# Kernel optimization log

Hardware: AMD Instinct MI355X
Metric: run time of the kernel (lower is better)

Reference implementation:

```python
import jax, jax.numpy as jnp
import numpy as np

EPS = 1e-8


def setup_inputs() -> dict:
    key = jax.random.key(0)
    k1, k2, k3, k4 = jax.random.split(key, 4)
    B, Cin, Cout, K, S, H, W = 8, 512, 512, 3, 512, 64, 64
    return {
        "x": jax.random.normal(k1, (B, Cin, H, W), dtype=jnp.float32),
        "style": jax.random.normal(k2, (B, S), dtype=jnp.float32),
        "weight": jax.random.normal(k3, (1, Cout, Cin, K, K), dtype=jnp.float32),
        "mod_w": jax.random.normal(k4, (Cin, S), dtype=jnp.float32),
        "mod_b": jnp.ones((Cin,), dtype=jnp.float32),
    }


def reference(x, style, weight, mod_w, mod_b):
    B, Cin, H, W = x.shape
    Cout, K = weight.shape[1], weight.shape[-1]
    style_dim = mod_w.shape[1]
    conv_scale = 1.0 / np.sqrt(Cin * K * K)  # 1/sqrt(fan_in)
    mod_scale = 1.0 / np.sqrt(style_dim)     # EqualLinear scale (lr_mul=1)

    # EqualLinear modulation: (B, Cin)
    s = style @ (mod_w * mod_scale).T + mod_b

    # per-sample modulated weights: (B, Cout, Cin, K, K)
    w = conv_scale * weight * s[:, None, :, None, None]
    demod = jax.lax.rsqrt(jnp.sum(w * w, axis=(2, 3, 4)) + EPS)  # (B, Cout)
    w = w * demod[:, :, None, None, None]

    # grouped conv with groups = batch
    w = w.reshape(B * Cout, Cin, K, K)
    xg = x.reshape(1, B * Cin, H, W)
    pad = (K - 1) // 2
    out = jax.lax.conv_general_dilated(
        xg, w,
        window_strides=(1, 1),
        padding=[(pad, pad), (pad, pad)],
        dimension_numbers=("NCHW", "OIHW", "NCHW"),
        feature_group_count=B,
    )
    return out.reshape(B, Cout, out.shape[2], out.shape[3])
```

## Files before the change

### kernel.cpp

```cpp
#include <hip/hip_runtime.h>
#include <hip/hip_bf16.h>
#include <cstdint>
#include <cstddef>

typedef __bf16 bf16x8 __attribute__((ext_vector_type(8)));
typedef float f32x4 __attribute__((ext_vector_type(4)));
typedef unsigned int uintx4 __attribute__((ext_vector_type(4)));

#define CONV_SCALE 0.014731391274719738f
#define MOD_SCALE  0.044194173824159216f

__device__ __forceinline__ unsigned short f2bf(float v) {
  unsigned int u = __float_as_uint(v);
  return (unsigned short)((u + 0x7FFFu + ((u >> 16) & 1u)) >> 16);
}

__device__ __forceinline__ void gload16(const void* g, void* l) {
  __builtin_amdgcn_global_load_lds(
      (const __attribute__((address_space(1))) unsigned int*)g,
      (__attribute__((address_space(3))) unsigned int*)l, 16, 0, 0);
}

__global__ void k_modulate(const float* __restrict__ style,
                           const float* __restrict__ mod_w,
                           const float* __restrict__ mod_b,
                           float* __restrict__ s) {
  int blk = blockIdx.x;
  int b = blk >> 2, ch = blk & 3;
  int t = threadIdx.x;
  int ci = ch * 128 + (t >> 1), half = t & 1;
  const float* st = style + b * 512 + half * 256;
  const float* mw = mod_w + (size_t)ci * 512 + half * 256;
  float acc = 0.f;
  #pragma unroll 8
  for (int k = 0; k < 256; k += 4) {
    f32x4 a = *(const f32x4*)(st + k);
    f32x4 m = *(const f32x4*)(mw + k);
    acc += a[0] * m[0] + a[1] * m[1] + a[2] * m[2] + a[3] * m[3];
  }
  acc += __shfl_xor(acc, 1);
  if (half == 0) s[b * 512 + ci] = acc * MOD_SCALE + mod_b[ci];
}

__global__ void k_wTq(const float* __restrict__ weight,
                      unsigned short* __restrict__ wT,
                      float* __restrict__ wsq) {
  __shared__ float lds[4608];
  int co = blockIdx.x;
  int t = threadIdx.x;
  const float* w = weight + (size_t)co * 4608;
  #pragma unroll
  for (int i = 0; i < 18; ++i) lds[t + i * 256] = w[t + i * 256];
  __syncthreads();
  for (int i = t; i < 576; i += 256) {
    int tap = i / 64, c8 = (i & 63) * 8;
    union { uintx4 v; unsigned short us[8]; } pk;
    #pragma unroll
    for (int j = 0; j < 8; ++j) pk.us[j] = f2bf(lds[(c8 + j) * 9 + tap]);
    *(uintx4*)(wT + ((size_t)tap * 512 + co) * 512 + c8) = pk.v;
  }
  for (int ci = t; ci < 512; ci += 256) {
    float a = 0.f;
    #pragma unroll
    for (int tap = 0; tap < 9; ++tap) { float v = lds[ci * 9 + tap]; a += v * v; }
    wsq[co * 512 + ci] = a * (CONV_SCALE * CONV_SCALE);
  }
}

__global__ void k_demod(const float* __restrict__ wsq, const float* __restrict__ s,
                        float* __restrict__ demod) {
  int b = blockIdx.x;
  int co = threadIdx.x;
  const float* wq = wsq + (size_t)co * 512;
  const float* sb = s + b * 512;
  float acc = 0.f;
  #pragma unroll 4
  for (int ci = 0; ci < 512; ci += 4) {
    f32x4 q = *(const f32x4*)(wq + ci);
    f32x4 v = *(const f32x4*)(sb + ci);
    acc += q[0] * v[0] * v[0] + q[1] * v[1] * v[1] + q[2] * v[2] * v[2] + q[3] * v[3] * v[3];
  }
  demod[b * 512 + co] = rsqrtf(acc + 1e-8f);
}

__global__ void k_xT(const float* __restrict__ x, const float* __restrict__ s,
                     unsigned short* __restrict__ xT) {
  __shared__ float lds[128][68];
  int cc = blockIdx.x;
  int h = blockIdx.y;
  int b = blockIdx.z;
  int t = threadIdx.x;
  int w4 = (t & 15) * 4, rr = t >> 4;
  #pragma unroll
  for (int i = 0; i < 8; ++i) {
    int ci = i * 16 + rr;
    *(f32x4*)&lds[ci][w4] =
        *(const f32x4*)&x[(((size_t)(b * 512 + cc * 128 + ci)) * 64 + h) * 64 + w4];
  }
  __syncthreads();
  int pos = t >> 2, c4 = t & 3;
  #pragma unroll
  for (int q = 0; q < 4; ++q) {
    int cb = q * 32 + c4 * 8;
    union { uintx4 v; unsigned short us[8]; } pk;
    #pragma unroll
    for (int j = 0; j < 8; ++j) {
      int ci = cb + j;
      pk.us[j] = f2bf(lds[ci][pos] * s[b * 512 + cc * 128 + ci]);
    }
    *(uintx4*)(xT + (((size_t)(b * 64 + h)) * 64 + pos) * 512 + cc * 128 + cb) = pk.v;
  }
}

__global__ __launch_bounds__(256, 2) void k_conv(
    const unsigned short* __restrict__ xT,
    const unsigned short* __restrict__ wT,
    const float* __restrict__ demod,
    float* __restrict__ out) {
  extern __shared__ __align__(16) char lds_raw[];
  char* xlds = lds_raw;
  char* wlds = lds_raw + 42240;

  const int co_t = blockIdx.x;
  const int h_t  = blockIdx.y;
  const int b    = blockIdx.z;
  const int t = threadIdx.x;
  const int lane = t & 63, wv = t >> 6;
  const int h0 = h_t * 8;
  const int co0 = co_t * 64;
  const int l15 = lane & 15, kg = lane >> 4;

  {
    uintx4 z = {0u, 0u, 0u, 0u};
    for (int i = t; i < 2640; i += 256) ((uintx4*)xlds)[i] = z;
  }

  f32x4 acc[4][2][4] = {};

  for (int cc = 0; cc < 16; ++cc) {
    __syncthreads();
    for (int j = wv; j < 40; j += 4) {
      int r = j >> 2, k = j & 3;
      int hh = h0 - 1 + r;
      if ((unsigned)hh < 64u) {
        int p0 = r * 66 + 1 + k * 16;
        int p = p0 + (lane >> 2);
        const unsigned short* g = xT + (((size_t)(b * 64 + hh)) * 64 + k * 16 + (lane >> 2)) * 512
                                  + cc * 32 + (((lane & 3) ^ ((p >> 1) & 3)) << 3);
        gload16(g, xlds + p0 * 64);
      }
    }
    for (int j = wv; j < 36; j += 4) {
      int row0 = j * 16;
      int row = row0 + (lane >> 2);
      int tap = row >> 6, co = row & 63;
      const unsigned short* g = wT + ((size_t)tap * 512 + co0 + co) * 512
                                + cc * 32 + (((lane & 3) ^ ((row >> 1) & 3)) << 3);
      gload16(g, wlds + row0 * 64);
    }
    __syncthreads();

    #pragma unroll
    for (int tap = 0; tap < 9; ++tap) {
      const int dh = tap / 3, dw = tap % 3;
      bf16x8 af[4], bfr[2][4];
      #pragma unroll
      for (int m = 0; m < 4; ++m) {
        int row = tap * 64 + m * 16 + l15;
        af[m] = *(const bf16x8*)(wlds + row * 64 + ((kg ^ ((row >> 1) & 3)) << 4));
      }
      #pragma unroll
      for (int r = 0; r < 2; ++r)
        #pragma unroll
        for (int n = 0; n < 4; ++n) {
          int p = (2 * wv + r + dh) * 66 + n * 16 + l15 + dw;
          bfr[r][n] = *(const bf16x8*)(xlds + p * 64 + ((kg ^ ((p >> 1) & 3)) << 4));
        }
      #pragma unroll
      for (int m = 0; m < 4; ++m)
        #pragma unroll
        for (int r = 0; r < 2; ++r)
          #pragma unroll
          for (int n = 0; n < 4; ++n)
            acc[m][r][n] = __builtin_amdgcn_mfma_f32_16x16x32_bf16(af[m], bfr[r][n], acc[m][r][n], 0, 0, 0);
    }
  }

  #pragma unroll
  for (int m = 0; m < 4; ++m) {
    #pragma unroll
    for (int q = 0; q < 4; ++q) {
      int co = co0 + m * 16 + kg * 4 + q;
      float scl = CONV_SCALE * demod[b * 512 + co];
      #pragma unroll
      for (int r = 0; r < 2; ++r) {
        int h_out = h0 + 2 * wv + r;
        #pragma unroll
        for (int n = 0; n < 4; ++n) {
          out[(((size_t)(b * 512 + co)) * 64 + h_out) * 64 + n * 16 + l15] = acc[m][r][n][q] * scl;
        }
      }
    }
  }
}

extern "C" void kernel_launch(void* const* d_in, const int* in_sizes, int n_in,
                              void* d_out, int out_size, void* d_ws, size_t ws_size,
                              hipStream_t stream) {
  const float* x      = (const float*)d_in[0];
  const float* style  = (const float*)d_in[1];
  const float* weight = (const float*)d_in[2];
  const float* mod_w  = (const float*)d_in[3];
  const float* mod_b  = (const float*)d_in[4];
  float* out = (float*)d_out;

  char* ws = (char*)d_ws;
  unsigned short* xT = (unsigned short*)ws;
  unsigned short* wT = (unsigned short*)(ws + 33554432);
  float* s     = (float*)(ws + 38273024);
  float* wsq   = (float*)(ws + 38289408);
  float* demod = (float*)(ws + 39337984);

  static int lds_set = 0;
  if (!lds_set) {
    (void)hipFuncSetAttribute((const void*)k_conv,
                              hipFuncAttributeMaxDynamicSharedMemorySize, 79104);
    lds_set = 1;
  }

  hipLaunchKernelGGL(k_modulate, dim3(32),       dim3(256), 0, stream, style, mod_w, mod_b, s);
  hipLaunchKernelGGL(k_wTq,      dim3(512),      dim3(256), 0, stream, weight, wT, wsq);
  hipLaunchKernelGGL(k_demod,    dim3(8),        dim3(512), 0, stream, wsq, s, demod);
  hipLaunchKernelGGL(k_xT,       dim3(4, 64, 8), dim3(256), 0, stream, x, s, xT);
  hipLaunchKernelGGL(k_conv,     dim3(8, 8, 8),  dim3(256), 79104, stream, xT, wT, demod, out);
}
```

Before: 193.9 us.

## Double-buffer conv tiles with register-staged prefetch and larger row tiles

The conv kernel now uses 512 threads covering 16 output rows per block, which halves the grid in h and doubles reuse of each weight tile. The next channel chunk is prefetched while the current one computes: x goes through registers and is written to LDS after compute, and weights are loaded asynchronously into a second LDS buffer. MFMA work runs at raised wave priority. LDS per block grows to about 146 KB, so only one block fits per CU despite the launch bound of two. Register pressure also rises from the nine staged x vectors, and the grid shrinks to 256 blocks.

```diff
diff --git a/kernel.cpp b/kernel.cpp
--- a/kernel.cpp
+++ b/kernel.cpp
@@ -112,54 +112,85 @@
   }
 }
 
-__global__ __launch_bounds__(256, 2) void k_conv(
+__global__ __launch_bounds__(512, 2) void k_conv(
     const unsigned short* __restrict__ xT,
     const unsigned short* __restrict__ wT,
     const float* __restrict__ demod,
     float* __restrict__ out) {
   extern __shared__ __align__(16) char lds_raw[];
   char* xlds = lds_raw;
-  char* wlds = lds_raw + 42240;
+  char* wlds = lds_raw + 76032;
 
   const int co_t = blockIdx.x;
   const int h_t  = blockIdx.y;
   const int b    = blockIdx.z;
   const int t = threadIdx.x;
   const int lane = t & 63, wv = t >> 6;
-  const int h0 = h_t * 8;
+  const int h0 = h_t * 16;
   const int co0 = co_t * 64;
   const int l15 = lane & 15, kg = lane >> 4;
 
   {
     uintx4 z = {0u, 0u, 0u, 0u};
-    for (int i = t; i < 2640; i += 256) ((uintx4*)xlds)[i] = z;
-  }
-
-  f32x4 acc[4][2][4] = {};
-
-  for (int cc = 0; cc < 16; ++cc) {
-    __syncthreads();
-    for (int j = wv; j < 40; j += 4) {
-      int r = j >> 2, k = j & 3;
-      int hh = h0 - 1 + r;
-      if ((unsigned)hh < 64u) {
-        int p0 = r * 66 + 1 + k * 16;
-        int p = p0 + (lane >> 2);
-        const unsigned short* g = xT + (((size_t)(b * 64 + hh)) * 64 + k * 16 + (lane >> 2)) * 512
-                                  + cc * 32 + (((lane & 3) ^ ((p >> 1) & 3)) << 3);
-        gload16(g, xlds + p0 * 64);
-      }
-    }
-    for (int j = wv; j < 36; j += 4) {
+    for (int i = t; i < 4752; i += 512) ((uintx4*)xlds)[i] = z;
+  }
+
+  const int slot = t & 3;
+  const int c    = (t >> 2) & 63;
+  const int rb   = t >> 8;
+  unsigned xgo[9]; unsigned xlo[9]; bool xv[9];
+  #pragma unroll
+  for (int k = 0; k < 9; ++k) {
+    int r = 2 * k + rb;
+    int hh = h0 - 1 + r;
+    xv[k] = ((unsigned)hh < 64u);
+    int p = r * 66 + 1 + c;
+    xlo[k] = p * 64 + ((slot ^ ((p >> 1) & 3)) << 4);
+    xgo[k] = ((unsigned)((b * 64 + (xv[k] ? hh : 0)) * 64 + c) << 10) + slot * 16;
+  }
+  const char* xTb = (const char*)xT;
+  uintx4 xr[9] = {};
+
+  auto xissue = [&](int ccn) {
+    unsigned off = ccn * 64;
+    #pragma unroll
+    for (int k = 0; k < 9; ++k)
+      if (xv[k]) xr[k] = *(const uintx4*)(xTb + xgo[k] + off);
+  };
+  auto xwrite = [&]() {
+    #pragma unroll
+    for (int k = 0; k < 9; ++k) *(uintx4*)(xlds + xlo[k]) = xr[k];
+  };
+  auto wissue = [&](int ccn, char* wb) {
+    for (int j = wv; j < 36; j += 8) {
       int row0 = j * 16;
       int row = row0 + (lane >> 2);
       int tap = row >> 6, co = row & 63;
       const unsigned short* g = wT + ((size_t)tap * 512 + co0 + co) * 512
-                                + cc * 32 + (((lane & 3) ^ ((row >> 1) & 3)) << 3);
-      gload16(g, wlds + row0 * 64);
-    }
-    __syncthreads();
-
+                                + ccn * 32 + (((lane & 3) ^ ((row >> 1) & 3)) << 3);
+      gload16(g, wb + row0 * 64);
+    }
+  };
+
+  f32x4 acc[4][2][4] = {};
+
+  char* wb0 = wlds;
+  char* wb1 = wlds + 36864;
+
+  xissue(0);
+  wissue(0, wb0);
+  xwrite();
+  __syncthreads();
+
+  #pragma unroll 1
+  for (int cc = 0; cc < 16; ++cc) {
+    char* wb = (cc & 1) ? wb1 : wb0;
+    if (cc < 15) {
+      xissue(cc + 1);
+      wissue(cc + 1, (cc & 1) ? wb0 : wb1);
+      __builtin_amdgcn_sched_barrier(0);
+    }
+    __builtin_amdgcn_s_setprio(1);
     #pragma unroll
     for (int tap = 0; tap < 9; ++tap) {
       const int dh = tap / 3, dw = tap % 3;
@@ -167,7 +198,7 @@
       #pragma unroll
       for (int m = 0; m < 4; ++m) {
         int row = tap * 64 + m * 16 + l15;
-        af[m] = *(const bf16x8*)(wlds + row * 64 + ((kg ^ ((row >> 1) & 3)) << 4));
+        af[m] = *(const bf16x8*)(wb + row * 64 + ((kg ^ ((row >> 1) & 3)) << 4));
       }
       #pragma unroll
       for (int r = 0; r < 2; ++r)
@@ -183,6 +214,12 @@
           #pragma unroll
           for (int n = 0; n < 4; ++n)
             acc[m][r][n] = __builtin_amdgcn_mfma_f32_16x16x32_bf16(af[m], bfr[r][n], acc[m][r][n], 0, 0, 0);
+    }
+    __builtin_amdgcn_s_setprio(0);
+    if (cc < 15) {
+      __syncthreads();
+      xwrite();
+      __syncthreads();
     }
   }
 
@@ -224,7 +261,7 @@
   static int lds_set = 0;
   if (!lds_set) {
     (void)hipFuncSetAttribute((const void*)k_conv,
-                              hipFuncAttributeMaxDynamicSharedMemorySize, 79104);
+                              hipFuncAttributeMaxDynamicSharedMemorySize, 149760);
     lds_set = 1;
   }
 
@@ -232,5 +269,5 @@
   hipLaunchKernelGGL(k_wTq,      dim3(512),      dim3(256), 0, stream, weight, wT, wsq);
   hipLaunchKernelGGL(k_demod,    dim3(8),        dim3(512), 0, stream, wsq, s, demod);
   hipLaunchKernelGGL(k_xT,       dim3(4, 64, 8), dim3(256), 0, stream, x, s, xT);
-  hipLaunchKernelGGL(k_conv,     dim3(8, 8, 8),  dim3(256), 79104, stream, xT, wT, demod, out);
-}
+  hipLaunchKernelGGL(k_conv,     dim3(8, 4, 8),  dim3(512), 149760, stream, xT, wT, demod, out);
+}
```

Result: slower. 269.6 us (+39.1%).

## Double-buffer conv input tiles and ring-buffer weights with 512-thread blocks

Applied to the files above, without the earlier changes.

Restructures the implicit-GEMM conv kernel into a software pipeline. The input tile is double-buffered, and weights stream per tap through a 4-slot LDS ring, with loads issued two taps ahead and gated by vmcnt waits instead of full barriers around each channel chunk. Blocks grow to 512 threads covering 128 output channels, which doubles input-tile reuse. A 1D grid reorders blocks by output-channel group, and s_setprio is raised around MFMA bursts. LDS use rises to about 118KB per block, which may limit occupancy to one block per CU. The hand-placed waitcnt counts and barrier placement are fragile.

```diff
diff --git a/kernel.cpp b/kernel.cpp
--- a/kernel.cpp
+++ b/kernel.cpp
@@ -112,70 +112,105 @@
   }
 }
 
-__global__ __launch_bounds__(256, 2) void k_conv(
+__global__ __launch_bounds__(512, 2) void k_conv(
     const unsigned short* __restrict__ xT,
     const unsigned short* __restrict__ wT,
     const float* __restrict__ demod,
     float* __restrict__ out) {
   extern __shared__ __align__(16) char lds_raw[];
-  char* xlds = lds_raw;
-  char* wlds = lds_raw + 42240;
-
-  const int co_t = blockIdx.x;
-  const int h_t  = blockIdx.y;
-  const int b    = blockIdx.z;
+  char* xb0   = lds_raw;
+  char* xb1   = lds_raw + 42240;
+  char* wring = lds_raw + 84480;
+  char* trash = lds_raw + 117248;
+
+  const int id  = blockIdx.x;
+  const int g_ord = (id & 7) * 32 + (id >> 3);
+  const int co_t  = g_ord >> 6;
+  const int slice = g_ord & 63;
+  const int b   = slice >> 3;
+  const int h_t = slice & 7;
+
   const int t = threadIdx.x;
   const int lane = t & 63, wv = t >> 6;
-  const int h0 = h_t * 8;
-  const int co0 = co_t * 64;
+  const int h0  = h_t * 8;
+  const int co0 = co_t * 128;
   const int l15 = lane & 15, kg = lane >> 4;
+  const int wrow = wv & 3;
+  const int wco  = wv >> 2;
 
   {
     uintx4 z = {0u, 0u, 0u, 0u};
-    for (int i = t; i < 2640; i += 256) ((uintx4*)xlds)[i] = z;
-  }
+    for (int i = t; i < 5280; i += 512) ((uintx4*)lds_raw)[i] = z;
+  }
+  __syncthreads();
+
+  auto xstage = [&](int j, int ccs, char* xbuf) {
+    int r = j >> 2, k = j & 3;
+    int hh = h0 - 1 + r;
+    int hc = ((unsigned)hh < 64u) ? hh : 0;
+    int p = r * 66 + 1 + k * 16 + (lane >> 2);
+    const void* src = xT + (((size_t)(b * 64 + hc)) * 64 + k * 16 + (lane >> 2)) * 512
+                      + ccs * 32 + (((lane & 3) ^ ((p >> 1) & 3)) << 3);
+    void* dst = ((unsigned)hh < 64u) ? (void*)(xbuf + (r * 66 + 1 + k * 16) * 64)
+                                     : (void*)trash;
+    gload16(src, dst);
+  };
+  auto wstage = [&](int g) {
+    int gc = (g <= 143) ? g : 143;
+    int s = g & 3;
+    int cc2 = gc / 9, tap2 = gc - cc2 * 9;
+    int row0 = wv * 16;
+    int row = row0 + (lane >> 2);
+    const void* src = wT + ((size_t)tap2 * 512 + co0 + row) * 512
+                      + cc2 * 32 + (((lane & 3) ^ ((row >> 1) & 3)) << 3);
+    void* dst = (g <= 143) ? (void*)(wring + s * 8192 + row0 * 64) : (void*)trash;
+    gload16(src, dst);
+  };
 
   f32x4 acc[4][2][4] = {};
 
+  #pragma unroll
+  for (int i = 0; i < 5; ++i) xstage(wv * 5 + i, 0, xb0);
+  wstage(0);
+  wstage(1);
+  __syncthreads();
+
+  #pragma unroll 1
   for (int cc = 0; cc < 16; ++cc) {
-    __syncthreads();
-    for (int j = wv; j < 40; j += 4) {
-      int r = j >> 2, k = j & 3;
-      int hh = h0 - 1 + r;
-      if ((unsigned)hh < 64u) {
-        int p0 = r * 66 + 1 + k * 16;
-        int p = p0 + (lane >> 2);
-        const unsigned short* g = xT + (((size_t)(b * 64 + hh)) * 64 + k * 16 + (lane >> 2)) * 512
-                                  + cc * 32 + (((lane & 3) ^ ((p >> 1) & 3)) << 3);
-        gload16(g, xlds + p0 * 64);
-      }
-    }
-    for (int j = wv; j < 36; j += 4) {
-      int row0 = j * 16;
-      int row = row0 + (lane >> 2);
-      int tap = row >> 6, co = row & 63;
-      const unsigned short* g = wT + ((size_t)tap * 512 + co0 + co) * 512
-                                + cc * 32 + (((lane & 3) ^ ((row >> 1) & 3)) << 3);
-      gload16(g, wlds + row0 * 64);
-    }
-    __syncthreads();
-
+    const char* xcur = (cc & 1) ? xb1 : xb0;
+    char* xnxt = (cc & 1) ? xb0 : xb1;
+    const int ccs = (cc + 1) & 15;
     #pragma unroll
     for (int tap = 0; tap < 9; ++tap) {
+      if (tap == 0 || tap == 1 || tap == 7 || tap == 8)
+        asm volatile("s_waitcnt vmcnt(1)" ::: "memory");
+      else
+        asm volatile("s_waitcnt vmcnt(2)" ::: "memory");
+
+      const int g = cc * 9 + tap;
+      const int s = g & 3;
       const int dh = tap / 3, dw = tap % 3;
+
       bf16x8 af[4], bfr[2][4];
       #pragma unroll
       for (int m = 0; m < 4; ++m) {
-        int row = tap * 64 + m * 16 + l15;
-        af[m] = *(const bf16x8*)(wlds + row * 64 + ((kg ^ ((row >> 1) & 3)) << 4));
+        int row = wco * 64 + m * 16 + l15;
+        af[m] = *(const bf16x8*)(wring + s * 8192 + row * 64 + ((kg ^ ((row >> 1) & 3)) << 4));
       }
       #pragma unroll
       for (int r = 0; r < 2; ++r)
         #pragma unroll
         for (int n = 0; n < 4; ++n) {
-          int p = (2 * wv + r + dh) * 66 + n * 16 + l15 + dw;
-          bfr[r][n] = *(const bf16x8*)(xlds + p * 64 + ((kg ^ ((p >> 1) & 3)) << 4));
+          int p = (2 * wrow + r + dh) * 66 + n * 16 + l15 + dw;
+          bfr[r][n] = *(const bf16x8*)(xcur + p * 64 + ((kg ^ ((p >> 1) & 3)) << 4));
         }
+
+      wstage(g + 2);
+      if (tap >= 1 && tap <= 5) xstage((tap - 1) * 8 + wv, ccs, xnxt);
+
+      __builtin_amdgcn_s_barrier();
+
+      __builtin_amdgcn_s_setprio(1);
       #pragma unroll
       for (int m = 0; m < 4; ++m)
         #pragma unroll
@@ -183,6 +218,7 @@
           #pragma unroll
           for (int n = 0; n < 4; ++n)
             acc[m][r][n] = __builtin_amdgcn_mfma_f32_16x16x32_bf16(af[m], bfr[r][n], acc[m][r][n], 0, 0, 0);
+      __builtin_amdgcn_s_setprio(0);
     }
   }
 
@@ -190,11 +226,11 @@
   for (int m = 0; m < 4; ++m) {
     #pragma unroll
     for (int q = 0; q < 4; ++q) {
-      int co = co0 + m * 16 + kg * 4 + q;
+      int co = co0 + wco * 64 + m * 16 + kg * 4 + q;
       float scl = CONV_SCALE * demod[b * 512 + co];
       #pragma unroll
       for (int r = 0; r < 2; ++r) {
-        int h_out = h0 + 2 * wv + r;
+        int h_out = h0 + 2 * wrow + r;
         #pragma unroll
         for (int n = 0; n < 4; ++n) {
           out[(((size_t)(b * 512 + co)) * 64 + h_out) * 64 + n * 16 + l15] = acc[m][r][n][q] * scl;
@@ -224,7 +260,7 @@
   static int lds_set = 0;
   if (!lds_set) {
     (void)hipFuncSetAttribute((const void*)k_conv,
-                              hipFuncAttributeMaxDynamicSharedMemorySize, 79104);
+                              hipFuncAttributeMaxDynamicSharedMemorySize, 118272);
     lds_set = 1;
   }
 
@@ -232,5 +268,5 @@
   hipLaunchKernelGGL(k_wTq,      dim3(512),      dim3(256), 0, stream, weight, wT, wsq);
   hipLaunchKernelGGL(k_demod,    dim3(8),        dim3(512), 0, stream, wsq, s, demod);
   hipLaunchKernelGGL(k_xT,       dim3(4, 64, 8), dim3(256), 0, stream, x, s, xT);
-  hipLaunchKernelGGL(k_conv,     dim3(8, 8, 8),  dim3(256), 79104, stream, xT, wT, demod, out);
-}
+  hipLaunchKernelGGL(k_conv,     dim3(256),      dim3(512), 118272, stream, xT, wT, demod, out);
+}
```

Result: faster. 183.2 us (-5.5%).
